# Kernel tuning notes

Measured on AMD Instinct MI355X. Metric: run time of the kernel, lower is better.

The kernel has to match this reference:

```python
import jax, jax.numpy as jnp
import numpy as np

B, C, H, W = 8, 512, 32, 32


def setup_inputs() -> dict:
    key = jax.random.key(0)
    ks = jax.random.split(key, 7)
    s = 0.02  # typical conv init scale
    return {
        "x": jax.random.normal(ks[0], (B, C, H, W), dtype=jnp.float32),
        "Wq": jax.random.normal(ks[1], (C, C), dtype=jnp.float32) * s,
        "bq": jax.random.normal(ks[2], (C,), dtype=jnp.float32) * s,
        "Wk": jax.random.normal(ks[3], (C, C), dtype=jnp.float32) * s,
        "bk": jax.random.normal(ks[4], (C,), dtype=jnp.float32) * s,
        "W6": jax.random.normal(ks[5], (C, C), dtype=jnp.float32) * s,
        "b6": jax.random.normal(ks[6], (C,), dtype=jnp.float32) * s,
    }


def _gam(x, Wq, bq, Wk, bk, W6, b6):
    b, c, h, w = x.shape
    hw = h * w
    scale = 1.0 / (c ** 0.5)
    # 1x1 convs == per-pixel channel matmuls (torch conv weight [out,in,1,1])
    q = jnp.einsum('bchw,dc->bhwd', x, Wq) + bq          # [B,H,W,C]
    q = q.reshape(b * hw, c)                              # query rows
    k = jnp.einsum('bchw,dc->bdhw', x, Wk) + bk[None, :, None, None]
    k = jnp.transpose(k, (1, 0, 2, 3)).reshape(c, b * hw)  # [C, B*HW]
    xw = (q.astype(jnp.float32) @ k.astype(jnp.float32))   # [B*HW, B*HW]
    xw = xw.reshape(b * hw, b, hw)
    xw = jnp.max(xw, axis=-1)                              # max over keys' spatial dim
    xw = jnp.mean(xw, axis=-1)                             # mean over key images
    xw = xw.reshape(b, hw) * scale
    xw = jax.nn.softmax(xw, axis=-1).astype(x.dtype)
    xw = xw.reshape(b, 1, h, w)
    x5 = x * xw
    return jnp.einsum('bchw,dc->bdhw', x5, W6) + b6[None, :, None, None]


def reference(x, Wq, bq, Wk, bk, W6, b6):
    x_new = _gam(x, Wq, bq, Wk, bk, W6, b6)
    # prototype: mean over batch and spatial dims, keep channels
    x_proto = jnp.mean(x_new.astype(jnp.float32), axis=(0, 2, 3)).astype(x.dtype)
    return x * x_proto[None, :, None, None]
```

## Files before the change

### kernel.cpp

```cpp
#include <hip/hip_runtime.h>
#include <hip/hip_bf16.h>

typedef __bf16 bf16_t;
typedef __bf16 bf16x8 __attribute__((ext_vector_type(8)));
typedef float f32x4 __attribute__((ext_vector_type(4)));

#define B_   8
#define C_   512
#define HW_  1024
#define NPIX 8192

typedef __attribute__((address_space(3))) void lds_vp;
typedef const __attribute__((address_space(1))) void gbl_vp;
__device__ __forceinline__ void gload_lds16(const void* g, void* l) {
    __builtin_amdgcn_global_load_lds((gbl_vp*)g, (lds_vp*)l, 16, 0, 0);
}

__device__ __forceinline__ void stage128x64(const bf16_t* __restrict__ g, int ldk,
                                            bf16_t* lds, int tid) {
    int w64 = tid & ~63;
#pragma unroll
    for (int s = 0; s < 4; ++s) {
        int u = s * 256 + tid;
        const bf16_t* src = g + (size_t)(u >> 3) * ldk + (u & 7) * 8;
        gload_lds16((const void*)src, (void*)(lds + (size_t)(s * 256 + w64) * 8));
    }
}

__global__ void k_cvt_w(const float* __restrict__ Wq, const float* __restrict__ Wk,
                        bf16_t* __restrict__ wq, bf16_t* __restrict__ wk) {
    int i = blockIdx.x * 256 + threadIdx.x;
    wq[i] = (bf16_t)Wq[i];
    wk[i] = (bf16_t)Wk[i];
}

__global__ void k_transpose(const float* __restrict__ x, bf16_t* __restrict__ xT) {
    __shared__ bf16_t tile[64 * 66];
    int p0 = blockIdx.x * 64, c0 = blockIdx.y * 64, b = blockIdx.z;
    int t = threadIdx.x;
#pragma unroll
    for (int s = 0; s < 16; ++s) {
        int u = s * 256 + t;
        int cr = u >> 6, pc = u & 63;
        tile[cr * 66 + pc] = (bf16_t)x[((size_t)(b * C_ + c0 + cr)) * HW_ + p0 + pc];
    }
    __syncthreads();
#pragma unroll
    for (int s = 0; s < 16; ++s) {
        int u = s * 256 + t;
        int pr = u >> 6, cc = u & 63;
        xT[((size_t)(b * HW_ + p0 + pr)) * C_ + c0 + cc] = tile[cc * 66 + pr];
    }
}

__launch_bounds__(256, 2)
__global__ void k_gemm_qk(const bf16_t* __restrict__ xT,
                          const bf16_t* __restrict__ wq, const bf16_t* __restrict__ wk,
                          const float* __restrict__ bq, const float* __restrict__ bk,
                          bf16_t* __restrict__ qo, bf16_t* __restrict__ ko) {
    __shared__ bf16_t As[128 * 64];
    __shared__ bf16_t Bs[128 * 64];
    int bid = blockIdx.x;
    int mtile = bid >> 3;
    int nt = bid & 7;
    const bf16_t* wsel = (nt < 4) ? wq : wk;
    const float*  bsel = (nt < 4) ? bq : bk;
    bf16_t*       osel = (nt < 4) ? qo : ko;
    int nb = (nt & 3) * 128;
    int i0 = mtile * 128;
    int tid = threadIdx.x;
    int lane = tid & 63, w = tid >> 6;
    int wr = w >> 1, wc = w & 1, lr = lane & 15, lg = lane >> 4;

    f32x4 acc[4][4];
#pragma unroll
    for (int mi = 0; mi < 4; ++mi)
#pragma unroll
        for (int ni = 0; ni < 4; ++ni)
#pragma unroll
            for (int r = 0; r < 4; ++r) acc[mi][ni][r] = 0.f;

    for (int kt = 0; kt < 8; ++kt) {
        int k0 = kt * 64;
        stage128x64(xT + (size_t)i0 * 512 + k0, 512, As, tid);
        stage128x64(wsel + (size_t)nb * 512 + k0, 512, Bs, tid);
        __syncthreads();
#pragma unroll
        for (int kk = 0; kk < 2; ++kk) {
            bf16x8 af[4], bfr[4];
#pragma unroll
            for (int mi = 0; mi < 4; ++mi)
                af[mi] = *reinterpret_cast<const bf16x8*>(
                    &As[(wr * 64 + mi * 16 + lr) * 64 + kk * 32 + lg * 8]);
#pragma unroll
            for (int ni = 0; ni < 4; ++ni)
                bfr[ni] = *reinterpret_cast<const bf16x8*>(
                    &Bs[(wc * 64 + ni * 16 + lr) * 64 + kk * 32 + lg * 8]);
#pragma unroll
            for (int mi = 0; mi < 4; ++mi)
#pragma unroll
                for (int ni = 0; ni < 4; ++ni)
                    acc[mi][ni] = __builtin_amdgcn_mfma_f32_16x16x32_bf16(
                        af[mi], bfr[ni], acc[mi][ni], 0, 0, 0);
        }
        __syncthreads();
    }
#pragma unroll
    for (int ni = 0; ni < 4; ++ni) {
        int col = nb + wc * 64 + ni * 16 + lr;
        float bias = bsel[col];
#pragma unroll
        for (int mi = 0; mi < 4; ++mi) {
            int rowb = i0 + wr * 64 + mi * 16 + lg * 4;
#pragma unroll
            for (int r = 0; r < 4; ++r)
                osel[(size_t)(rowb + r) * 512 + col] = (bf16_t)(acc[mi][ni][r] + bias);
        }
    }
}


#define STAGE_A(RH, D, T)                                                          \
    gload_lds16((const void*)(q + srcA + (size_t)((RH) * 128) * 512 +              \
                              ((T) & 7) * 64),                                     \
                (void*)(ldsb + (RH) * 32768 + (D) * 16384 + ldw));                 \
    gload_lds16((const void*)(q + srcA + (size_t)((RH) * 128 + 64) * 512 +         \
                              ((T) & 7) * 64),                                     \
                (void*)(ldsb + (RH) * 32768 + (D) * 16384 + 8192 + ldw));

#define STAGE_B(RH, D, T)                                                          \
    gload_lds16((const void*)(kb + srcB +                                          \
                              (size_t)(((T) >> 3) * 256 + (RH) * 128) * 512 +      \
                              ((T) & 7) * 64),                                     \
                (void*)(ldsb + 65536 + (RH) * 32768 + (D) * 16384 + ldw));         \
    gload_lds16((const void*)(kb + srcB +                                          \
                              (size_t)(((T) >> 3) * 256 + (RH) * 128 + 64) * 512 + \
                              ((T) & 7) * 64),                                     \
                (void*)(ldsb + 65536 + (RH) * 32768 + (D) * 16384 + 8192 + ldw));

#define PHASE(D, KH, MH, STAGE_STMT, VM_STMT)                                      \
    {                                                                              \
        const char* Ab = ldsb + wr * 32768 + (D) * 16384;                          \
        const char* Bb = ldsb + 65536 + (wc >> 1) * 32768 + (D) * 16384;           \
        _Pragma("unroll")                                                          \
        for (int mi = 0; mi < 4; ++mi)                                             \
            af[mi] = *(const bf16x8*)(Ab + (aswz ^ ((KH) * 64)) +                  \
                                      ((MH) * 4 + mi) * 2048);                     \
        if ((MH) == 0) {                                                           \
            _Pragma("unroll")                                                      \
            for (int ni = 0; ni < 4; ++ni)                                         \
                bf[ni] = *(const bf16x8*)(Bb + (bswz ^ ((KH) * 64)) + ni * 2048);  \
        }                                                                          \
        STAGE_STMT;                                                                \
        __builtin_amdgcn_s_setprio(1);                                             \
        _Pragma("unroll")                                                          \
        for (int mi = 0; mi < 4; ++mi)                                             \
            _Pragma("unroll")                                                      \
            for (int ni = 0; ni < 4; ++ni)                                         \
                acc[(MH) * 4 + mi][ni] = __builtin_amdgcn_mfma_f32_16x16x32_bf16(  \
                    af[mi], bf[ni], acc[(MH) * 4 + mi][ni], 0, 0, 0);              \
        __builtin_amdgcn_s_setprio(0);                                             \
        VM_STMT;                                                                   \
        __builtin_amdgcn_s_barrier();                                              \
    }

__global__ __launch_bounds__(512, 2)
void k_gemm_max8(const bf16_t* __restrict__ q, const bf16_t* __restrict__ kp,
                 float* __restrict__ Mout) {
    __shared__ __align__(16) bf16_t lds[65536];
    char* ldsb = (char*)lds;
    int bid = blockIdx.x;
    int img = bid & 7;
    int qp = bid >> 3;
    int i0 = qp * 256;
    const bf16_t* kb = kp + (size_t)img * HW_ * C_;
    int tid = threadIdx.x;
    int lane = tid & 63, w = tid >> 6;
    int wr = w >> 2, wc = w & 3;
    int lr = lane & 15, lg = lane >> 4;
    int kswz = (lg ^ (lr & 7)) << 4;
    int aswz = lr * 128 + kswz;
    int bswz = ((wc & 1) * 64 + lr) * 128 + kswz;

    int srow = tid >> 3;
    int sk = (((tid & 7) ^ ((tid >> 3) & 7))) << 3;
    size_t srcA = (size_t)(i0 + srow) * 512 + sk;
    size_t srcB = (size_t)srow * 512 + sk;
    int ldw = (tid >> 6) * 1024;

    f32x4 acc[8][4];
    bf16x8 af[4], bf[4];
    float rm[8][4];
#pragma unroll
    for (int mi = 0; mi < 8; ++mi)
#pragma unroll
        for (int ni = 0; ni < 4; ++ni)
#pragma unroll
            for (int r = 0; r < 4; ++r) acc[mi][ni][r] = 0.f;
#pragma unroll
    for (int mi = 0; mi < 8; ++mi)
#pragma unroll
        for (int r = 0; r < 4; ++r) rm[mi][r] = -3.4e38f;

    STAGE_B(0, 0, 0) STAGE_A(0, 0, 0) STAGE_B(1, 0, 0) STAGE_A(1, 0, 0)
    STAGE_B(0, 1, 1)
    asm volatile("s_waitcnt vmcnt(2)" ::: "memory");
    __builtin_amdgcn_s_barrier();

    for (int i = 0; i < 16; ++i) {
        int tb = 2 * i + 1, tc = 2 * i + 2, td = 2 * i + 3;
        bool s = (i < 15);
        PHASE(0, 0, 0, { STAGE_A(0, 1, tb) }, {})
        PHASE(0, 0, 1, { STAGE_B(1, 1, tb) }, {})
        PHASE(0, 1, 0, { STAGE_A(1, 1, tb) }, {})
        PHASE(0, 1, 1, { if (s) { STAGE_B(0, 0, tc) } },
              { if (s) { asm volatile("s_waitcnt vmcnt(2)" ::: "memory"); }
                else   { asm volatile("s_waitcnt vmcnt(0)" ::: "memory"); } })
        PHASE(1, 0, 0, { if (s) { STAGE_A(0, 0, tc) } }, {})
        PHASE(1, 0, 1, { if (s) { STAGE_B(1, 0, tc) } }, {})
        PHASE(1, 1, 0, { if (s) { STAGE_A(1, 0, tc) } }, {})
        PHASE(1, 1, 1, { if (s) { STAGE_B(0, 1, td) } },
              { if (s) { asm volatile("s_waitcnt vmcnt(2)" ::: "memory"); } })
        if ((i & 3) == 3) {
#pragma unroll
            for (int mi = 0; mi < 8; ++mi)
#pragma unroll
                for (int r = 0; r < 4; ++r) {
                    float v = fmaxf(fmaxf(acc[mi][0][r], acc[mi][1][r]),
                                    fmaxf(acc[mi][2][r], acc[mi][3][r]));
                    rm[mi][r] = fmaxf(rm[mi][r], v);
#pragma unroll
                    for (int ni = 0; ni < 4; ++ni) acc[mi][ni][r] = 0.f;
                }
        }
    }

#pragma unroll
    for (int mi = 0; mi < 8; ++mi)
#pragma unroll
        for (int r = 0; r < 4; ++r) {
            float v = rm[mi][r];
#pragma unroll
            for (int off = 1; off < 16; off <<= 1) v = fmaxf(v, __shfl_xor(v, off));
            rm[mi][r] = v;
        }
    float* sm = (float*)lds;
    if (lr == 0) {
#pragma unroll
        for (int mi = 0; mi < 8; ++mi)
#pragma unroll
            for (int r = 0; r < 4; ++r)
                sm[wc * 256 + wr * 128 + mi * 16 + lg * 4 + r] = rm[mi][r];
    }
    __syncthreads();
    if (tid < 256) {
        float v = fmaxf(fmaxf(sm[tid], sm[256 + tid]),
                        fmaxf(sm[512 + tid], sm[768 + tid]));
        Mout[(size_t)(i0 + tid) * 8 + img] = v;
    }
}

__global__ void k_softmax(const float* __restrict__ Mout, float* __restrict__ wsm) {
    int b = blockIdx.x;
    int t = threadIdx.x;
    __shared__ float red[16];
    const float scale = 0.044194173824159216f;
    float s[4];
#pragma unroll
    for (int i = 0; i < 4; ++i) {
        int p = t + i * 256;
        const float* row = &Mout[(size_t)(b * 1024 + p) * 8];
        float acc = 0.f;
#pragma unroll
        for (int j = 0; j < 8; ++j) acc += row[j];
        s[i] = acc * (scale / 8.0f);
    }
    float m = fmaxf(fmaxf(s[0], s[1]), fmaxf(s[2], s[3]));
#pragma unroll
    for (int off = 1; off < 64; off <<= 1) m = fmaxf(m, __shfl_xor(m, off));
    if ((t & 63) == 0) red[t >> 6] = m;
    __syncthreads();
    float m4 = fmaxf(fmaxf(red[0], red[1]), fmaxf(red[2], red[3]));
    float e[4], sum = 0.f;
#pragma unroll
    for (int i = 0; i < 4; ++i) { e[i] = __expf(s[i] - m4); sum += e[i]; }
#pragma unroll
    for (int off = 1; off < 64; off <<= 1) sum += __shfl_xor(sum, off);
    if ((t & 63) == 0) red[8 + (t >> 6)] = sum;
    __syncthreads();
    float tot = red[8] + red[9] + red[10] + red[11];
    float inv = 1.0f / tot;
#pragma unroll
    for (int i = 0; i < 4; ++i) wsm[b * 1024 + t + i * 256] = e[i] * inv;
}

__global__ void k_reduce_y(const float* __restrict__ x, const float* __restrict__ wsm,
                           float* __restrict__ y) {
    int c = blockIdx.x;
    int t = threadIdx.x;
    float acc = 0.f;
    for (int b = 0; b < 8; ++b) {
        const float* xb = x + ((size_t)(b * C_ + c)) * HW_;
        const float* wb = wsm + b * HW_;
#pragma unroll
        for (int i = 0; i < 4; ++i) {
            int p = t + i * 256;
            acc += xb[p] * wb[p];
        }
    }
#pragma unroll
    for (int off = 1; off < 64; off <<= 1) acc += __shfl_xor(acc, off);
    __shared__ float red[4];
    if ((t & 63) == 0) red[t >> 6] = acc;
    __syncthreads();
    if (t == 0) y[c] = (red[0] + red[1] + red[2] + red[3]) * (1.0f / 8192.0f);
}

__global__ void k_proto(const float* __restrict__ W6, const float* __restrict__ b6,
                        const float* __restrict__ y, float* __restrict__ proto) {
    int d = blockIdx.x;
    int lane = threadIdx.x;
    float acc = 0.f;
#pragma unroll
    for (int i = 0; i < 8; ++i)
        acc += W6[(size_t)d * C_ + lane + i * 64] * y[lane + i * 64];
#pragma unroll
    for (int off = 1; off < 64; off <<= 1) acc += __shfl_xor(acc, off);
    if (lane == 0) proto[d] = acc + b6[d];
}

__global__ void k_final(const float* __restrict__ x, const float* __restrict__ proto,
                        float* __restrict__ out) {
    int idx = blockIdx.x * 256 + threadIdx.x;
    float4 v = ((const float4*)x)[idx];
    int c = (idx >> 8) & 511;
    float p = proto[c];
    v.x *= p; v.y *= p; v.z *= p; v.w *= p;
    ((float4*)out)[idx] = v;
}

extern "C" void kernel_launch(void* const* d_in, const int* in_sizes, int n_in,
                              void* d_out, int out_size, void* d_ws, size_t ws_size,
                              hipStream_t stream) {
    const float* x  = (const float*)d_in[0];
    const float* Wq = (const float*)d_in[1];
    const float* bq = (const float*)d_in[2];
    const float* Wk = (const float*)d_in[3];
    const float* bk = (const float*)d_in[4];
    const float* W6 = (const float*)d_in[5];
    const float* b6 = (const float*)d_in[6];
    float* out = (float*)d_out;

    char* ws = (char*)d_ws;
    bf16_t* xT    = (bf16_t*)(ws);
    float*  Mout  = (float*)(ws);
    bf16_t* wqb   = (bf16_t*)(ws + 8388608);
    bf16_t* wkb   = (bf16_t*)(ws + 8912896);
    bf16_t* qb    = (bf16_t*)(ws + 9437184);
    bf16_t* kb    = (bf16_t*)(ws + 17825792);
    float*  wsm   = (float*)(ws + 26476544);
    float*  yv    = (float*)(ws + 26509312);
    float*  proto = (float*)(ws + 26511360);

    hipLaunchKernelGGL(k_cvt_w, dim3(1024), dim3(256), 0, stream, Wq, Wk, wqb, wkb);
    hipLaunchKernelGGL(k_transpose, dim3(16, 8, 8), dim3(256), 0, stream, x, xT);
    hipLaunchKernelGGL(k_gemm_qk, dim3(512), dim3(256), 0, stream,
                       xT, wqb, wkb, bq, bk, qb, kb);
    hipLaunchKernelGGL(k_gemm_max8, dim3(256), dim3(512), 0, stream, qb, kb, Mout);
    hipLaunchKernelGGL(k_softmax, dim3(8), dim3(256), 0, stream, Mout, wsm);
    hipLaunchKernelGGL(k_reduce_y, dim3(512), dim3(256), 0, stream, x, wsm, yv);
    hipLaunchKernelGGL(k_proto, dim3(512), dim3(64), 0, stream, W6, b6, yv, proto);
    hipLaunchKernelGGL(k_final, dim3(4096), dim3(256), 0, stream, x, proto, out);
}
```

Baseline: 103.2 us.

## Double-buffer LDS fragment registers to overlap reads with MFMA in GEMM-max

Restructures the main GEMM loop so each phase reads the next phase's A/B fragments from LDS into a second register set while running MFMAs on the current set. The global-to-LDS staging schedule is reordered so B halves are issued together, with vmcnt(0) waits placed before the buffer flip. The aim is to hide ds_read latency behind matrix instructions. In exchange it uses more VGPRs, which under launch_bounds(512,2) could cause spills, and the full vmcnt(0) waits may expose global load latency.

After: 103.0 us. Within noise of the previous version (-0.2%).

```diff
diff --git a/kernel.cpp b/kernel.cpp
--- a/kernel.cpp
+++ b/kernel.cpp
@@ -138,29 +138,30 @@
                               ((T) & 7) * 64),                                     \
                 (void*)(ldsb + 65536 + (RH) * 32768 + (D) * 16384 + 8192 + ldw));
 
-#define PHASE(D, KH, MH, STAGE_STMT, VM_STMT)                                      \
+#define PHASE(RSET, RD, RKH, RMH, RBF, RBSET, CSET, CMH, CBSET, STG, VM)           \
     {                                                                              \
-        const char* Ab = ldsb + wr * 32768 + (D) * 16384;                          \
-        const char* Bb = ldsb + 65536 + (wc >> 1) * 32768 + (D) * 16384;           \
+        const char* rAb = ldsb + wr * 32768 + (RD) * 16384;                        \
         _Pragma("unroll")                                                          \
         for (int mi = 0; mi < 4; ++mi)                                             \
-            af[mi] = *(const bf16x8*)(Ab + (aswz ^ ((KH) * 64)) +                  \
-                                      ((MH) * 4 + mi) * 2048);                     \
-        if ((MH) == 0) {                                                           \
+            af[RSET][mi] = *(const bf16x8*)(rAb + (aswz ^ ((RKH) * 64)) +          \
+                                            ((RMH) * 4 + mi) * 2048);              \
+        if (RBF) {                                                                 \
+            const char* rBb = ldsb + 65536 + (wc >> 1) * 32768 + (RD) * 16384;     \
             _Pragma("unroll")                                                      \
             for (int ni = 0; ni < 4; ++ni)                                         \
-                bf[ni] = *(const bf16x8*)(Bb + (bswz ^ ((KH) * 64)) + ni * 2048);  \
+                bf[RBSET][ni] = *(const bf16x8*)(rBb + (bswz ^ ((RKH) * 64)) +     \
+                                                 ni * 2048);                       \
         }                                                                          \
-        STAGE_STMT;                                                                \
+        STG;                                                                       \
         __builtin_amdgcn_s_setprio(1);                                             \
         _Pragma("unroll")                                                          \
         for (int mi = 0; mi < 4; ++mi)                                             \
             _Pragma("unroll")                                                      \
             for (int ni = 0; ni < 4; ++ni)                                         \
-                acc[(MH) * 4 + mi][ni] = __builtin_amdgcn_mfma_f32_16x16x32_bf16(  \
-                    af[mi], bf[ni], acc[(MH) * 4 + mi][ni], 0, 0, 0);              \
+                acc[(CMH) * 4 + mi][ni] = __builtin_amdgcn_mfma_f32_16x16x32_bf16( \
+                    af[CSET][mi], bf[CBSET][ni], acc[(CMH) * 4 + mi][ni], 0, 0, 0);\
         __builtin_amdgcn_s_setprio(0);                                             \
-        VM_STMT;                                                                   \
+        VM;                                                                        \
         __builtin_amdgcn_s_barrier();                                              \
     }
 
@@ -189,7 +190,7 @@
     int ldw = (tid >> 6) * 1024;
 
     f32x4 acc[8][4];
-    bf16x8 af[4], bf[4];
+    bf16x8 af[2][4], bf[2][4];
     float rm[8][4];
 #pragma unroll
     for (int mi = 0; mi < 8; ++mi)
@@ -202,25 +203,36 @@
 #pragma unroll
         for (int r = 0; r < 4; ++r) rm[mi][r] = -3.4e38f;
 
-    STAGE_B(0, 0, 0) STAGE_A(0, 0, 0) STAGE_B(1, 0, 0) STAGE_A(1, 0, 0)
-    STAGE_B(0, 1, 1)
-    asm volatile("s_waitcnt vmcnt(2)" ::: "memory");
+    STAGE_B(0, 0, 0) STAGE_B(1, 0, 0) STAGE_A(0, 0, 0) STAGE_A(1, 0, 0)
+    STAGE_B(0, 1, 1) STAGE_B(1, 1, 1)
+    asm volatile("s_waitcnt vmcnt(4)" ::: "memory");
     __builtin_amdgcn_s_barrier();
+    {
+        const char* rAb = ldsb + wr * 32768;
+#pragma unroll
+        for (int mi = 0; mi < 4; ++mi)
+            af[0][mi] = *(const bf16x8*)(rAb + aswz + mi * 2048);
+        const char* rBb = ldsb + 65536 + (wc >> 1) * 32768;
+#pragma unroll
+        for (int ni = 0; ni < 4; ++ni)
+            bf[0][ni] = *(const bf16x8*)(rBb + bswz + ni * 2048);
+    }
 
     for (int i = 0; i < 16; ++i) {
         int tb = 2 * i + 1, tc = 2 * i + 2, td = 2 * i + 3;
         bool s = (i < 15);
-        PHASE(0, 0, 0, { STAGE_A(0, 1, tb) }, {})
-        PHASE(0, 0, 1, { STAGE_B(1, 1, tb) }, {})
-        PHASE(0, 1, 0, { STAGE_A(1, 1, tb) }, {})
-        PHASE(0, 1, 1, { if (s) { STAGE_B(0, 0, tc) } },
-              { if (s) { asm volatile("s_waitcnt vmcnt(2)" ::: "memory"); }
-                else   { asm volatile("s_waitcnt vmcnt(0)" ::: "memory"); } })
-        PHASE(1, 0, 0, { if (s) { STAGE_A(0, 0, tc) } }, {})
-        PHASE(1, 0, 1, { if (s) { STAGE_B(1, 0, tc) } }, {})
-        PHASE(1, 1, 0, { if (s) { STAGE_A(1, 0, tc) } }, {})
-        PHASE(1, 1, 1, { if (s) { STAGE_B(0, 1, td) } },
-              { if (s) { asm volatile("s_waitcnt vmcnt(2)" ::: "memory"); } })
+        PHASE(1, 0, 0, 1, 0, 0,  0, 0, 0, { STAGE_A(0, 1, tb) }, {})
+        PHASE(0, 0, 1, 0, 1, 1,  1, 1, 0, { STAGE_A(1, 1, tb) }, {})
+        PHASE(1, 0, 1, 1, 0, 0,  0, 0, 1, {},
+              { asm volatile("s_waitcnt vmcnt(0)" ::: "memory"); })
+        PHASE(0, 1, 0, 0, 1, 0,  1, 1, 1,
+              { if (s) { STAGE_B(0, 0, tc) STAGE_B(1, 0, tc) } }, {})
+        PHASE(1, 1, 0, 1, 0, 0,  0, 0, 0, { if (s) { STAGE_A(0, 0, tc) } }, {})
+        PHASE(0, 1, 1, 0, 1, 1,  1, 1, 0, { if (s) { STAGE_A(1, 0, tc) } }, {})
+        PHASE(1, 1, 1, 1, 0, 0,  0, 0, 1, {},
+              { asm volatile("s_waitcnt vmcnt(0)" ::: "memory"); })
+        PHASE(0, 0, 0, 0, 1, 0,  1, 1, 1,
+              { if (s) { STAGE_B(0, 1, td) STAGE_B(1, 1, td) } }, {})
         if ((i & 3) == 3) {
 #pragma unroll
             for (int mi = 0; mi < 8; ++mi)
```
